# Optimization experiments

Measured on AMD Instinct MI355X. Metric: run time of the kernel, lower is better.

## Reference

```python
import jax, jax.numpy as jnp
import numpy as np
import math

B, S, H = 2, 2048, 2048
NQ, NKV, HD = 16, 4, 128
THETA = 10000.0


def rotate_half(x):
    x1, x2 = jnp.split(x, 2, axis=-1)
    return jnp.concatenate([-x2, x1], axis=-1)


def rope_cos_sin(position_ids, dim, base, dtype):
    # inv_freq: (dim/2,)
    inv_freq = 1.0 / (base ** (jnp.arange(0, dim, 2, dtype=jnp.float32) / dim))
    freqs = position_ids.astype(jnp.float32)[..., None] * inv_freq  # (B, S, dim/2)
    emb = jnp.concatenate([freqs, freqs], axis=-1)  # (B, S, dim)
    return jnp.cos(emb).astype(dtype), jnp.sin(emb).astype(dtype)


def setup_inputs() -> dict:
    key = jax.random.key(0)
    ks = jax.random.split(key, 5)
    hidden_states = jax.random.normal(ks[0], (B, S, H), dtype=jnp.float32)
    position_ids = jnp.broadcast_to(jnp.arange(S, dtype=jnp.int32)[None, :], (B, S))
    sc = 0.02
    wq = jax.random.normal(ks[1], (NQ * HD, H), dtype=jnp.float32) * sc
    wk = jax.random.normal(ks[2], (NKV * HD, H), dtype=jnp.float32) * sc
    wv = jax.random.normal(ks[3], (NKV * HD, H), dtype=jnp.float32) * sc
    wo = jax.random.normal(ks[4], (H, NQ * HD), dtype=jnp.float32) * sc
    return {"hidden_states": hidden_states, "position_ids": position_ids,
            "wq": wq, "wk": wk, "wv": wv, "wo": wo}


def reference(hidden_states, position_ids, wq, wk, wv, wo):
    b, s, _ = hidden_states.shape
    n_rep = NQ // NKV
    # QKV projections (no bias)
    q = (hidden_states @ wq.T).reshape(b, s, NQ, HD).transpose(0, 2, 1, 3)   # (b, nq, s, hd)
    k = (hidden_states @ wk.T).reshape(b, s, NKV, HD).transpose(0, 2, 1, 3)  # (b, nkv, s, hd)
    v = (hidden_states @ wv.T).reshape(b, s, NKV, HD).transpose(0, 2, 1, 3)
    # RoPE (full rotary, partial_rotary_factor == 1.0)
    cos, sin = rope_cos_sin(position_ids, HD, THETA, q.dtype)  # (b, s, hd)
    cos = cos[:, None, :, :]
    sin = sin[:, None, :, :]
    q = q * cos + rotate_half(q) * sin
    k = k * cos + rotate_half(k) * sin
    # repeat_kv for GQA: (b, nkv, s, hd) -> (b, nq, s, hd)
    k = jnp.repeat(k, n_rep, axis=1)
    v = jnp.repeat(v, n_rep, axis=1)
    # scores (b, nq, s, s)
    scores = jnp.einsum('bhqd,bhkd->bhqk', q, k) / math.sqrt(HD)
    causal = jnp.triu(jnp.full((s, s), -jnp.inf, dtype=scores.dtype), k=1)
    scores = scores + causal
    probs = jax.nn.softmax(scores.astype(jnp.float32), axis=-1).astype(q.dtype)
    out = jnp.einsum('bhqk,bhkd->bhqd', probs, v)  # (b, nq, s, hd)
    out = out.transpose(0, 2, 1, 3).reshape(b, s, NQ * HD)
    return out @ wo.T
```

## Files before the change

kernel.cpp:

```cpp
#include <hip/hip_runtime.h>
#include <hip/hip_bf16.h>
#include <cstdint>

typedef unsigned short u16;
typedef __attribute__((ext_vector_type(4))) float f32x4;
typedef __attribute__((ext_vector_type(8))) short s16x8;
typedef __attribute__((ext_vector_type(4))) unsigned int u32x4;
typedef __attribute__((ext_vector_type(2))) unsigned int u32x2;
typedef __attribute__((ext_vector_type(4))) unsigned short u16x4;
typedef __attribute__((ext_vector_type(8))) unsigned short u16x8;

#define MFMA16(a, b, c) __builtin_amdgcn_mfma_f32_16x16x32_bf16(a, b, c, 0, 0, 0)
#define GLOAD16(g, l) __builtin_amdgcn_global_load_lds((const __attribute__((address_space(1))) void*)(g), (__attribute__((address_space(3))) void*)(l), 16, 0, 0)

__device__ __forceinline__ u16 f2bf(float f) {
    union { float f; uint32_t u; } v{f};
    uint32_t r = v.u + 0x7FFF + ((v.u >> 16) & 1);
    return (u16)(r >> 16);
}
__device__ __forceinline__ float bf2f(u16 b) {
    union { uint32_t u; float f; } v;
    v.u = ((uint32_t)b) << 16;
    return v.f;
}

__global__ void cast_all(const float* __restrict__ h, const float* __restrict__ wq,
                         const float* __restrict__ wk, const float* __restrict__ wv,
                         const float* __restrict__ wo, const int* __restrict__ pos,
                         u16* __restrict__ Xb, u16* __restrict__ WB, u16* __restrict__ WoB,
                         float* __restrict__ ct, float* __restrict__ st) {
    if (blockIdx.x >= 18432) {
        int i = (blockIdx.x - 18432) * 256 + threadIdx.x;
        int j = i & 63;
        int bs = i >> 6;
        float p = (float)pos[bs];
        float invf = powf(10000.0f, -(float)j * (1.0f / 64.0f));
        float ang = p * invf;
        ct[i] = cosf(ang);
        st[i] = sinf(ang);
        return;
    }
    int i = blockIdx.x * 256 + threadIdx.x;
    const float* src; u16* dst; int off;
    if (i < 2097152)      { src = h;  dst = Xb;           off = i; }
    else if (i < 3145728) { src = wq; dst = WB;           off = i - 2097152; }
    else if (i < 3407872) { src = wk; dst = WB + 4194304; off = i - 3145728; }
    else if (i < 3670016) { src = wv; dst = WB + 5242880; off = i - 3407872; }
    else                  { src = wo; dst = WoB;          off = i - 3670016; }
    float4 f = ((const float4*)src)[off];
    u16x4 o = { f2bf(f.x), f2bf(f.y), f2bf(f.z), f2bf(f.w) };
    ((u16x4*)dst)[off] = o;
}

template <int FUSE>
__global__ __launch_bounds__(256) void gemm_bt(const u16* __restrict__ A, const u16* __restrict__ Bw,
                                               float* __restrict__ C, int M, int N, int K,
                                               const float* __restrict__ ct, const float* __restrict__ st,
                                               u16* __restrict__ Qb, u16* __restrict__ Kb,
                                               u16* __restrict__ Vb) {
    __shared__ u16 Sh[32768];
    const int tid = threadIdx.x;
    const int lane = tid & 63, wid = tid >> 6;
    const int g = lane >> 4, r = lane & 15;

    const int gx = gridDim.x, nwg = gx * gridDim.y;
    int lid = blockIdx.y * gx + blockIdx.x;
    int swz = (lid % 8) * (nwg / 8) + lid / 8;
    const int bxi = swz % gx, byi = swz / gx;

    const size_t bm = (size_t)byi * 128, bn = (size_t)bxi * 128;
    const int wr = (wid >> 1) * 64, wc = (wid & 1) * 64;

    const int srow = wid * 32 + (lane >> 3);
    const int schunk = (lane & 7) ^ ((lane >> 3) & 7);
    const u16* aSrc = A + (bm + srow) * (size_t)K + schunk * 8;
    const u16* bSrc = Bw + (bn + srow) * (size_t)K + schunk * 8;

    auto STAGE = [&](int ktEl, int bi) {
        u16* aD = Sh + bi * 16384 + wid * 2048;
        u16* bD = Sh + bi * 16384 + 8192 + wid * 2048;
#pragma unroll
        for (int j = 0; j < 4; ++j) {
            GLOAD16(aSrc + (size_t)(j * 8) * K + ktEl, aD + j * 512);
            GLOAD16(bSrc + (size_t)(j * 8) * K + ktEl, bD + j * 512);
        }
    };

    f32x4 acc[4][4] = {};
    const int nk = K >> 6;
    STAGE(0, 0);
    __syncthreads();
    for (int t = 0; t < nk; ++t) {
        if (t + 1 < nk) STAGE((t + 1) << 6, (t + 1) & 1);
        const u16* As = Sh + (t & 1) * 16384;
        const u16* Bs = As + 8192;
        s16x8 af[4][2], bfr[4][2];
#pragma unroll
        for (int m = 0; m < 4; ++m)
#pragma unroll
            for (int kk = 0; kk < 2; ++kk) {
                int rowa = wr + m * 16 + r;
                af[m][kk] = *(const s16x8*)(As + rowa * 64 + (((kk * 4 + g) ^ (rowa & 7)) << 3));
                int rowb = wc + m * 16 + r;
                bfr[m][kk] = *(const s16x8*)(Bs + rowb * 64 + (((kk * 4 + g) ^ (rowb & 7)) << 3));
            }
#pragma unroll
        for (int m = 0; m < 4; ++m)
#pragma unroll
            for (int n = 0; n < 4; ++n) {
                acc[m][n] = MFMA16(af[m][0], bfr[n][0], acc[m][n]);
                acc[m][n] = MFMA16(af[m][1], bfr[n][1], acc[m][n]);
            }
        __syncthreads();
    }
    if (FUSE == 0) {
#pragma unroll
        for (int m = 0; m < 4; ++m)
#pragma unroll
            for (int n = 0; n < 4; ++n)
#pragma unroll
                for (int i = 0; i < 4; ++i) {
                    size_t row = bm + wr + m * 16 + g * 4 + i;
                    size_t col = bn + wc + n * 16 + r;
                    C[row * N + col] = acc[m][n][i];
                }
        return;
    }
    const int hb = bxi;
    if (hb < 20) {
#pragma unroll
        for (int m = 0; m < 4; ++m)
#pragma unroll
            for (int n = 0; n < 4; ++n)
#pragma unroll
                for (int i = 0; i < 4; ++i) {
                    int rowl = wr + m * 16 + g * 4 + i;
                    int col = wc + n * 16 + r;
                    int c4 = col >> 3;
                    *(u16*)((char*)Sh + rowl * 256 + (((c4 ^ (rowl & 15))) << 4) + ((col & 7) << 1)) =
                        f2bf(acc[m][n][i]);
                }
        __syncthreads();
        if (tid < 128) {
            const int rowl = tid;
            const size_t tok = bm + rowl;
            const int b = (int)(tok >> 11), s = (int)(tok & 2047);
            u16* dst;
            if (hb < 16) dst = Qb + (((size_t)(b * 16 + hb) * 2048 + s) << 7);
            else         dst = Kb + (((size_t)(b * 4 + (hb - 16)) * 2048 + s) << 7);
            const char* tb = (const char*)Sh + rowl * 256;
            const float* ctr = ct + tok * 64;
            const float* str = st + tok * 64;
#pragma unroll
            for (int c4 = 0; c4 < 8; ++c4) {
                u32x4 lo4 = *(const u32x4*)(tb + ((c4 ^ (rowl & 15)) << 4));
                u32x4 hi4 = *(const u32x4*)(tb + (((c4 + 8) ^ (rowl & 15)) << 4));
                const u16* lo = (const u16*)&lo4;
                const u16* hi = (const u16*)&hi4;
                u16x4 o0, o1, o2, o3;
                u16* olo[2] = { (u16*)&o0, (u16*)&o1 };
                u16* ohi[2] = { (u16*)&o2, (u16*)&o3 };
#pragma unroll
                for (int j = 0; j < 8; ++j) {
                    float c = ctr[c4 * 8 + j], sn = str[c4 * 8 + j];
                    float xl = bf2f(lo[j]), xh = bf2f(hi[j]);
                    olo[j >> 2][j & 3] = f2bf(xl * c - xh * sn);
                    ohi[j >> 2][j & 3] = f2bf(xh * c + xl * sn);
                }
                *(u16x4*)(dst + c4 * 8) = o0;
                *(u16x4*)(dst + c4 * 8 + 4) = o1;
                *(u16x4*)(dst + 64 + c4 * 8) = o2;
                *(u16x4*)(dst + 64 + c4 * 8 + 4) = o3;
            }
        }
    } else {
#pragma unroll
        for (int m = 0; m < 4; ++m) {
            int tokb = wr + m * 16 + g * 4;
            int chunk = tokb >> 3;
            int sub = (g & 1) * 8;
#pragma unroll
            for (int n = 0; n < 4; ++n) {
                int d = wc + n * 16 + r;
                u16x4 v = { f2bf(acc[m][n][0]), f2bf(acc[m][n][1]),
                            f2bf(acc[m][n][2]), f2bf(acc[m][n][3]) };
                *(u16x4*)((char*)Sh + d * 256 + (((chunk ^ (d & 15))) << 4) + sub) = v;
            }
        }
        __syncthreads();
        const int b = (int)(bm >> 11), s0 = (int)(bm & 2047);
        u16* dst = Vb + (size_t)(b * 4 + (hb - 20)) * 262144;
        const int dd = tid >> 1, half = (tid & 1) * 8;
#pragma unroll
        for (int c8 = 0; c8 < 8; ++c8) {
            int sc = half + c8;
            u32x4 v4 = *(const u32x4*)((const char*)Sh + dd * 256 + (((sc ^ (dd & 15))) << 4));
            *(u32x4*)(dst + (size_t)dd * 2048 + s0 + sc * 8) = v4;
        }
    }
}

__global__ __launch_bounds__(256, 2) void attn_k(const u16* __restrict__ Qb, const u16* __restrict__ Kb,
                                                 const u16* __restrict__ Vb, u16* __restrict__ Ob) {
    __shared__ char smem[65536];
    u16* Vts = (u16*)(smem + 32768);
    char* Pall = smem + 49152;
    const int tid = threadIdx.x;
    const int lane = tid & 63, w = tid >> 6;
    const int g = lane >> 4, r = lane & 15;

    const int lid = blockIdx.y * gridDim.x + blockIdx.x;
    const int cpy = lid >> 8, p = lid & 255;
    const int bh = p & 31;
    const int qblk = cpy ? (7 - (p >> 5)) : ((p >> 5) + 8);

    const int b = bh >> 4, h = bh & 15;
    const int hkv = h >> 2;
    const int q0 = qblk * 128;
    const u16* Qh = Qb + ((size_t)(b * 16 + h) << 18);
    const u16* Kh = Kb + ((size_t)(b * 4 + hkv) << 18);
    const u16* Vh = Vb + ((size_t)(b * 4 + hkv) << 18);

    s16x8 qf[2][4];
#pragma unroll
    for (int qq = 0; qq < 2; ++qq)
#pragma unroll
        for (int c = 0; c < 4; ++c)
            qf[qq][c] = *(const s16x8*)(Qh + (size_t)(q0 + qq * 64 + w * 16 + r) * 128 + c * 32 + g * 8);

    f32x4 o[2][8] = {};
    float mrun[2] = {-1e30f, -1e30f};
    float lrun[2] = {0.f, 0.f};
    const int fmax[2] = { q0 + w * 16 + 15, q0 + 64 + w * 16 + 15 };

    const int ntiles = 2 * qblk + 2;
    const int krow0 = tid >> 4, kch = tid & 15;

    u32x4 kpr[4], vpr[4];
#pragma unroll
    for (int it = 0; it < 4; ++it)
        kpr[it] = *(const u32x4*)(Kh + (size_t)(krow0 + it * 16) * 128 + kch * 8);
#pragma unroll
    for (int it = 0; it < 4; ++it) {
        int task = tid + it * 256;
        vpr[it] = *(const u32x4*)(Vh + (size_t)(task >> 3) * 2048 + (task & 7) * 8);
    }
#pragma unroll
    for (int it = 0; it < 4; ++it) {
        int row = krow0 + it * 16;
        *(u32x4*)(smem + row * 256 + ((kch ^ (row & 7)) << 4)) = kpr[it];
    }
#pragma unroll
    for (int it = 0; it < 4; ++it) {
        int task = tid + it * 256;
        int d = task >> 3, ch = task & 7;
        *(u32x4*)((char*)Vts + d * 128 + ((ch ^ (d & 7) ^ ((d >> 3) & 7)) << 4)) = vpr[it];
    }
    if (ntiles > 1) {
#pragma unroll
        for (int it = 0; it < 4; ++it)
            kpr[it] = *(const u32x4*)(Kh + (size_t)(64 + krow0 + it * 16) * 128 + kch * 8);
#pragma unroll
        for (int it = 0; it < 4; ++it) {
            int task = tid + it * 256;
            vpr[it] = *(const u32x4*)(Vh + (size_t)(task >> 3) * 2048 + 64 + (task & 7) * 8);
        }
    }
    __syncthreads();

    for (int t = 0; t < ntiles; ++t) {
        const int kv0 = t * 64;
        const char* kb = smem + ((t & 1) << 14);
        f32x4 st4[2][4];
#pragma unroll
        for (int ts = 0; ts < 4; ++ts) {
            int row = ts * 16 + r;
            s16x8 kf[4];
#pragma unroll
            for (int c = 0; c < 4; ++c)
                kf[c] = *(const s16x8*)(kb + row * 256 + (((c * 4 + g) ^ (row & 7)) << 4));
            f32x4 a0 = {}, a1 = {};
            if (kv0 <= fmax[0])
#pragma unroll
                for (int c = 0; c < 4; ++c) a0 = MFMA16(kf[c], qf[0][c], a0);
            if (kv0 <= fmax[1])
#pragma unroll
                for (int c = 0; c < 4; ++c) a1 = MFMA16(kf[c], qf[1][c], a1);
            st4[0][ts] = a0;
            st4[1][ts] = a1;
        }
#pragma unroll
        for (int qq = 0; qq < 2; ++qq) {
            if (kv0 > fmax[qq]) continue;
            const int qg = q0 + qq * 64 + w * 16 + r;
            float sv[16];
            float mtile = -1e30f;
#pragma unroll
            for (int ts = 0; ts < 4; ++ts)
#pragma unroll
                for (int i = 0; i < 4; ++i) {
                    int kvg = kv0 + ts * 16 + g * 4 + i;
                    float s = st4[qq][ts][i] * 0.08838834764831845f;
                    s = (kvg > qg) ? -1e30f : s;
                    sv[ts * 4 + i] = s;
                    mtile = fmaxf(mtile, s);
                }
            mtile = fmaxf(mtile, __shfl_xor(mtile, 16));
            mtile = fmaxf(mtile, __shfl_xor(mtile, 32));
            float mold = mrun[qq];
            if (!__all(mtile <= mold + 8.0f)) {
                float mnew = fmaxf(mold, mtile);
                float corr = __expf(mold - mnew);
#pragma unroll
                for (int dsb = 0; dsb < 8; ++dsb)
#pragma unroll
                    for (int i = 0; i < 4; ++i) o[qq][dsb][i] *= corr;
                lrun[qq] *= corr;
                mrun[qq] = mnew;
            }
            float mm = mrun[qq];
            float psum = 0.f;
            unsigned int pw[8];
#pragma unroll
            for (int ts = 0; ts < 4; ++ts) {
                float p0 = __expf(sv[ts * 4 + 0] - mm);
                float p1 = __expf(sv[ts * 4 + 1] - mm);
                float p2 = __expf(sv[ts * 4 + 2] - mm);
                float p3 = __expf(sv[ts * 4 + 3] - mm);
                psum += (p0 + p1) + (p2 + p3);
                pw[ts * 2 + 0] = (unsigned int)f2bf(p0) | ((unsigned int)f2bf(p1) << 16);
                pw[ts * 2 + 1] = (unsigned int)f2bf(p2) | ((unsigned int)f2bf(p3) << 16);
            }
            psum += __shfl_xor(psum, 16);
            psum += __shfl_xor(psum, 32);
            lrun[qq] += psum;
            char* pbase = Pall + (w * 2 + qq) * 2048;
#pragma unroll
            for (int ts = 0; ts < 4; ++ts) {
                int chunk = (ts * 2 + (g >> 1)) ^ (r & 7);
                u32x2 val = { pw[ts * 2], pw[ts * 2 + 1] };
                *(u32x2*)(pbase + r * 128 + chunk * 16 + (g & 1) * 8) = val;
            }
        }
        asm volatile("s_waitcnt lgkmcnt(0)" ::: "memory");
        if (t + 1 < ntiles) {
            char* kbn = smem + (((t + 1) & 1) << 14);
#pragma unroll
            for (int it = 0; it < 4; ++it) {
                int row = krow0 + it * 16;
                *(u32x4*)(kbn + row * 256 + ((kch ^ (row & 7)) << 4)) = kpr[it];
            }
            if (t + 2 < ntiles) {
                const int kn2 = kv0 + 128;
#pragma unroll
                for (int it = 0; it < 4; ++it)
                    kpr[it] = *(const u32x4*)(Kh + (size_t)(kn2 + krow0 + it * 16) * 128 + kch * 8);
            }
        }
#pragma unroll
        for (int c = 0; c < 2; ++c) {
            s16x8 vf[8];
#pragma unroll
            for (int dsb = 0; dsb < 8; ++dsb) {
                int d = dsb * 16 + r;
                vf[dsb] = *(const s16x8*)((const char*)Vts + d * 128 +
                    ((((c * 4 + g) ^ (d & 7) ^ ((d >> 3) & 7))) << 4));
            }
#pragma unroll
            for (int qq = 0; qq < 2; ++qq) {
                if (kv0 > fmax[qq]) continue;
                s16x8 pf = *(const s16x8*)(Pall + (w * 2 + qq) * 2048 + r * 128 +
                                           (((c * 4 + g) ^ (r & 7)) << 4));
#pragma unroll
                for (int dsb = 0; dsb < 8; ++dsb)
                    o[qq][dsb] = MFMA16(vf[dsb], pf, o[qq][dsb]);
            }
        }
        __syncthreads();
        if (t + 1 < ntiles) {
#pragma unroll
            for (int it = 0; it < 4; ++it) {
                int task = tid + it * 256;
                int d = task >> 3, ch = task & 7;
                *(u32x4*)((char*)Vts + d * 128 + ((ch ^ (d & 7) ^ ((d >> 3) & 7)) << 4)) = vpr[it];
            }
            if (t + 2 < ntiles) {
                const int kn2 = kv0 + 128;
#pragma unroll
                for (int it = 0; it < 4; ++it) {
                    int task = tid + it * 256;
                    vpr[it] = *(const u32x4*)(Vh + (size_t)(task >> 3) * 2048 + kn2 + (task & 7) * 8);
                }
            }
        }
        __syncthreads();
    }
#pragma unroll
    for (int qq = 0; qq < 2; ++qq) {
        float linv = 1.0f / lrun[qq];
        char* obase = smem + (w << 13) + (qq << 12);
#pragma unroll
        for (int dsb = 0; dsb < 8; ++dsb)
#pragma unroll
            for (int i = 0; i < 4; ++i) {
                int d = dsb * 16 + g * 4 + i;
                *(u16*)(obase + r * 256 + d * 2) = f2bf(o[qq][dsb][i] * linv);
            }
    }
    asm volatile("s_waitcnt lgkmcnt(0)" ::: "memory");
    const int rr = lane >> 2, cbo = (lane & 3) * 32;
#pragma unroll
    for (int qq = 0; qq < 2; ++qq) {
        char* obase = smem + (w << 13) + (qq << 12);
        size_t oidx = ((size_t)b * 2048 + q0 + qq * 64 + w * 16 + rr) * 2048 + h * 128 + cbo;
#pragma unroll
        for (int p2 = 0; p2 < 4; ++p2) {
            u32x4 vv = *(const u32x4*)(obase + rr * 256 + cbo * 2 + p2 * 16);
            *(u32x4*)(Ob + oidx + p2 * 8) = vv;
        }
    }
}

extern "C" void kernel_launch(void* const* d_in, const int* in_sizes, int n_in,
                              void* d_out, int out_size, void* d_ws, size_t ws_size,
                              hipStream_t stream) {
    const float* hidden = (const float*)d_in[0];
    const int* pos = (const int*)d_in[1];
    const float* wq = (const float*)d_in[2];
    const float* wk = (const float*)d_in[3];
    const float* wv = (const float*)d_in[4];
    const float* wo = (const float*)d_in[5];
    float* out = (float*)d_out;

    char* ws = (char*)d_ws;
    size_t off = 0;
    auto alloc = [&](size_t bytes) { char* p = ws + off; off += (bytes + 255) & ~255ULL; return p; };
    u16* Xb   = (u16*)alloc(8388608ULL * 2);
    u16* WB   = (u16*)alloc(6291456ULL * 2);
    u16* WoB  = (u16*)alloc(4194304ULL * 2);
    u16* Qb   = (u16*)alloc(8388608ULL * 2);
    u16* Kb   = (u16*)alloc(2097152ULL * 2);
    u16* Vb   = (u16*)alloc(2097152ULL * 2);
    u16* Ab   = (u16*)alloc(8388608ULL * 2);
    float* ctab = (float*)alloc(262144ULL * 4);
    float* stab = (float*)alloc(262144ULL * 4);

    cast_all<<<19456, 256, 0, stream>>>(hidden, wq, wk, wv, wo, pos, Xb, WB, WoB, ctab, stab);
    gemm_bt<1><<<dim3(24, 32), 256, 0, stream>>>(Xb, WB, nullptr, 4096, 3072, 2048,
                                                 ctab, stab, Qb, Kb, Vb);
    attn_k<<<dim3(16, 32), 256, 0, stream>>>(Qb, Kb, Vb, Ab);
    gemm_bt<0><<<dim3(16, 32), 256, 0, stream>>>(Ab, WoB, out, 4096, 2048, 2048,
                                                 nullptr, nullptr, nullptr, nullptr, nullptr);
}
```

Measured before the change: 229.4 us.

## Enlarge attention blocks to 512 threads covering 256 query rows

The attention kernel now runs 8 waves per block, each block covering 256 query rows instead of 128. Each K/V tile staged in shared memory is therefore reused by twice as many query rows, and the grid is halved to 256 blocks. The P·V step is moved inside the per-query-group loop, so V fragments are re-read from LDS for each group, and the next K-tile store is interleaved into that loop. The old scheme pairing complementary causal query blocks for load balance is dropped, so blocks now differ widely in the number of KV tiles they process, and occupancy drops to one block per CU.

```diff
diff --git a/kernel.cpp b/kernel.cpp
--- a/kernel.cpp
+++ b/kernel.cpp
@@ -200,7 +200,7 @@
     }
 }
 
-__global__ __launch_bounds__(256, 2) void attn_k(const u16* __restrict__ Qb, const u16* __restrict__ Kb,
+__global__ __launch_bounds__(512, 1) void attn_k(const u16* __restrict__ Qb, const u16* __restrict__ Kb,
                                                  const u16* __restrict__ Vb, u16* __restrict__ Ob) {
     __shared__ char smem[65536];
     u16* Vts = (u16*)(smem + 32768);
@@ -210,59 +210,60 @@
     const int g = lane >> 4, r = lane & 15;
 
     const int lid = blockIdx.y * gridDim.x + blockIdx.x;
-    const int cpy = lid >> 8, p = lid & 255;
-    const int bh = p & 31;
-    const int qblk = cpy ? (7 - (p >> 5)) : ((p >> 5) + 8);
+    const int bh = lid & 31;
+    const int qblk = 7 - (lid >> 5);
 
     const int b = bh >> 4, h = bh & 15;
     const int hkv = h >> 2;
-    const int q0 = qblk * 128;
+    const int q0 = qblk * 256;
     const u16* Qh = Qb + ((size_t)(b * 16 + h) << 18);
     const u16* Kh = Kb + ((size_t)(b * 4 + hkv) << 18);
     const u16* Vh = Vb + ((size_t)(b * 4 + hkv) << 18);
 
+    const int base0 = q0 + w * 16, base1 = q0 + 128 + w * 16;
+    const int fmax[2] = { base0 + 15, base1 + 15 };
+
     s16x8 qf[2][4];
 #pragma unroll
-    for (int qq = 0; qq < 2; ++qq)
-#pragma unroll
-        for (int c = 0; c < 4; ++c)
-            qf[qq][c] = *(const s16x8*)(Qh + (size_t)(q0 + qq * 64 + w * 16 + r) * 128 + c * 32 + g * 8);
+    for (int c = 0; c < 4; ++c) {
+        qf[0][c] = *(const s16x8*)(Qh + (size_t)(base0 + r) * 128 + c * 32 + g * 8);
+        qf[1][c] = *(const s16x8*)(Qh + (size_t)(base1 + r) * 128 + c * 32 + g * 8);
+    }
 
     f32x4 o[2][8] = {};
     float mrun[2] = {-1e30f, -1e30f};
     float lrun[2] = {0.f, 0.f};
-    const int fmax[2] = { q0 + w * 16 + 15, q0 + 64 + w * 16 + 15 };
-
-    const int ntiles = 2 * qblk + 2;
+
+    const int ntiles = 4 * qblk + 4;
     const int krow0 = tid >> 4, kch = tid & 15;
 
-    u32x4 kpr[4], vpr[4];
-#pragma unroll
-    for (int it = 0; it < 4; ++it)
-        kpr[it] = *(const u32x4*)(Kh + (size_t)(krow0 + it * 16) * 128 + kch * 8);
-#pragma unroll
-    for (int it = 0; it < 4; ++it) {
-        int task = tid + it * 256;
+    u32x4 kpr[2], vpr[2];
+#pragma unroll
+    for (int it = 0; it < 2; ++it)
+        kpr[it] = *(const u32x4*)(Kh + (size_t)(krow0 + it * 32) * 128 + kch * 8);
+#pragma unroll
+    for (int it = 0; it < 2; ++it) {
+        int task = tid + it * 512;
         vpr[it] = *(const u32x4*)(Vh + (size_t)(task >> 3) * 2048 + (task & 7) * 8);
     }
 #pragma unroll
-    for (int it = 0; it < 4; ++it) {
-        int row = krow0 + it * 16;
+    for (int it = 0; it < 2; ++it) {
+        int row = krow0 + it * 32;
         *(u32x4*)(smem + row * 256 + ((kch ^ (row & 7)) << 4)) = kpr[it];
     }
 #pragma unroll
-    for (int it = 0; it < 4; ++it) {
-        int task = tid + it * 256;
+    for (int it = 0; it < 2; ++it) {
+        int task = tid + it * 512;
         int d = task >> 3, ch = task & 7;
         *(u32x4*)((char*)Vts + d * 128 + ((ch ^ (d & 7) ^ ((d >> 3) & 7)) << 4)) = vpr[it];
     }
     if (ntiles > 1) {
 #pragma unroll
-        for (int it = 0; it < 4; ++it)
-            kpr[it] = *(const u32x4*)(Kh + (size_t)(64 + krow0 + it * 16) * 128 + kch * 8);
-#pragma unroll
-        for (int it = 0; it < 4; ++it) {
-            int task = tid + it * 256;
+        for (int it = 0; it < 2; ++it)
+            kpr[it] = *(const u32x4*)(Kh + (size_t)(64 + krow0 + it * 32) * 128 + kch * 8);
+#pragma unroll
+        for (int it = 0; it < 2; ++it) {
+            int task = tid + it * 512;
             vpr[it] = *(const u32x4*)(Vh + (size_t)(task >> 3) * 2048 + 64 + (task & 7) * 8);
         }
     }
@@ -291,104 +292,97 @@
         }
 #pragma unroll
         for (int qq = 0; qq < 2; ++qq) {
-            if (kv0 > fmax[qq]) continue;
-            const int qg = q0 + qq * 64 + w * 16 + r;
-            float sv[16];
-            float mtile = -1e30f;
-#pragma unroll
-            for (int ts = 0; ts < 4; ++ts)
-#pragma unroll
-                for (int i = 0; i < 4; ++i) {
-                    int kvg = kv0 + ts * 16 + g * 4 + i;
-                    float s = st4[qq][ts][i] * 0.08838834764831845f;
-                    s = (kvg > qg) ? -1e30f : s;
-                    sv[ts * 4 + i] = s;
-                    mtile = fmaxf(mtile, s);
-                }
-            mtile = fmaxf(mtile, __shfl_xor(mtile, 16));
-            mtile = fmaxf(mtile, __shfl_xor(mtile, 32));
-            float mold = mrun[qq];
-            if (!__all(mtile <= mold + 8.0f)) {
-                float mnew = fmaxf(mold, mtile);
-                float corr = __expf(mold - mnew);
-#pragma unroll
-                for (int dsb = 0; dsb < 8; ++dsb)
-#pragma unroll
-                    for (int i = 0; i < 4; ++i) o[qq][dsb][i] *= corr;
-                lrun[qq] *= corr;
-                mrun[qq] = mnew;
-            }
-            float mm = mrun[qq];
-            float psum = 0.f;
-            unsigned int pw[8];
-#pragma unroll
-            for (int ts = 0; ts < 4; ++ts) {
-                float p0 = __expf(sv[ts * 4 + 0] - mm);
-                float p1 = __expf(sv[ts * 4 + 1] - mm);
-                float p2 = __expf(sv[ts * 4 + 2] - mm);
-                float p3 = __expf(sv[ts * 4 + 3] - mm);
-                psum += (p0 + p1) + (p2 + p3);
-                pw[ts * 2 + 0] = (unsigned int)f2bf(p0) | ((unsigned int)f2bf(p1) << 16);
-                pw[ts * 2 + 1] = (unsigned int)f2bf(p2) | ((unsigned int)f2bf(p3) << 16);
-            }
-            psum += __shfl_xor(psum, 16);
-            psum += __shfl_xor(psum, 32);
-            lrun[qq] += psum;
-            char* pbase = Pall + (w * 2 + qq) * 2048;
-#pragma unroll
-            for (int ts = 0; ts < 4; ++ts) {
-                int chunk = (ts * 2 + (g >> 1)) ^ (r & 7);
-                u32x2 val = { pw[ts * 2], pw[ts * 2 + 1] };
-                *(u32x2*)(pbase + r * 128 + chunk * 16 + (g & 1) * 8) = val;
-            }
-        }
-        asm volatile("s_waitcnt lgkmcnt(0)" ::: "memory");
+            if (kv0 <= fmax[qq]) {
+                const int qg = (qq ? base1 : base0) + r;
+                float sv[16];
+                float mtile = -1e30f;
+#pragma unroll
+                for (int ts = 0; ts < 4; ++ts)
+#pragma unroll
+                    for (int i = 0; i < 4; ++i) {
+                        int kvg = kv0 + ts * 16 + g * 4 + i;
+                        float s = st4[qq][ts][i] * 0.08838834764831845f;
+                        s = (kvg > qg) ? -1e30f : s;
+                        sv[ts * 4 + i] = s;
+                        mtile = fmaxf(mtile, s);
+                    }
+                mtile = fmaxf(mtile, __shfl_xor(mtile, 16));
+                mtile = fmaxf(mtile, __shfl_xor(mtile, 32));
+                float mold = mrun[qq];
+                if (!__all(mtile <= mold + 8.0f)) {
+                    float mnew = fmaxf(mold, mtile);
+                    float corr = __expf(mold - mnew);
+#pragma unroll
+                    for (int dsb = 0; dsb < 8; ++dsb)
+#pragma unroll
+                        for (int i = 0; i < 4; ++i) o[qq][dsb][i] *= corr;
+                    lrun[qq] *= corr;
+                    mrun[qq] = mnew;
+                }
+                float mm = mrun[qq];
+                float psum = 0.f;
+                unsigned int pw[8];
+#pragma unroll
+                for (int ts = 0; ts < 4; ++ts) {
+                    float p0 = __expf(sv[ts * 4 + 0] - mm);
+                    float p1 = __expf(sv[ts * 4 + 1] - mm);
+                    float p2 = __expf(sv[ts * 4 + 2] - mm);
+                    float p3 = __expf(sv[ts * 4 + 3] - mm);
+                    psum += (p0 + p1) + (p2 + p3);
+                    pw[ts * 2 + 0] = (unsigned int)f2bf(p0) | ((unsigned int)f2bf(p1) << 16);
+                    pw[ts * 2 + 1] = (unsigned int)f2bf(p2) | ((unsigned int)f2bf(p3) << 16);
+                }
+                psum += __shfl_xor(psum, 16);
+                psum += __shfl_xor(psum, 32);
+                lrun[qq] += psum;
+                char* pbase = Pall + w * 2048;
+#pragma unroll
+                for (int ts = 0; ts < 4; ++ts) {
+                    int chunk = (ts * 2 + (g >> 1)) ^ (r & 7);
+                    u32x2 val = { pw[ts * 2], pw[ts * 2 + 1] };
+                    *(u32x2*)(pbase + r * 128 + chunk * 16 + (g & 1) * 8) = val;
+                }
+                asm volatile("s_waitcnt lgkmcnt(0)" ::: "memory");
+#pragma unroll
+                for (int c = 0; c < 2; ++c) {
+                    s16x8 pf = *(const s16x8*)(pbase + r * 128 + (((c * 4 + g) ^ (r & 7)) << 4));
+#pragma unroll
+                    for (int dsb = 0; dsb < 8; ++dsb) {
+                        int d = dsb * 16 + r;
+                        s16x8 vf = *(const s16x8*)((const char*)Vts + d * 128 +
+                            ((((c * 4 + g) ^ (d & 7) ^ ((d >> 3) & 7))) << 4));
+                        o[qq][dsb] = MFMA16(vf, pf, o[qq][dsb]);
+                    }
+                }
+            }
+            if (qq == 0 && t + 1 < ntiles) {
+                char* kbn = smem + (((t + 1) & 1) << 14);
+#pragma unroll
+                for (int it = 0; it < 2; ++it) {
+                    int row = krow0 + it * 32;
+                    *(u32x4*)(kbn + row * 256 + ((kch ^ (row & 7)) << 4)) = kpr[it];
+                }
+                if (t + 2 < ntiles) {
+                    const int kn2 = kv0 + 128;
+#pragma unroll
+                    for (int it = 0; it < 2; ++it)
+                        kpr[it] = *(const u32x4*)(Kh + (size_t)(kn2 + krow0 + it * 32) * 128 + kch * 8);
+                }
+            }
+        }
+        __syncthreads();
         if (t + 1 < ntiles) {
-            char* kbn = smem + (((t + 1) & 1) << 14);
-#pragma unroll
-            for (int it = 0; it < 4; ++it) {
-                int row = krow0 + it * 16;
-                *(u32x4*)(kbn + row * 256 + ((kch ^ (row & 7)) << 4)) = kpr[it];
+#pragma unroll
+            for (int it = 0; it < 2; ++it) {
+                int task = tid + it * 512;
+                int d = task >> 3, ch = task & 7;
+                *(u32x4*)((char*)Vts + d * 128 + ((ch ^ (d & 7) ^ ((d >> 3) & 7)) << 4)) = vpr[it];
             }
             if (t + 2 < ntiles) {
                 const int kn2 = kv0 + 128;
 #pragma unroll
-                for (int it = 0; it < 4; ++it)
-                    kpr[it] = *(const u32x4*)(Kh + (size_t)(kn2 + krow0 + it * 16) * 128 + kch * 8);
-            }
-        }
-#pragma unroll
-        for (int c = 0; c < 2; ++c) {
-            s16x8 vf[8];
-#pragma unroll
-            for (int dsb = 0; dsb < 8; ++dsb) {
-                int d = dsb * 16 + r;
-                vf[dsb] = *(const s16x8*)((const char*)Vts + d * 128 +
-                    ((((c * 4 + g) ^ (d & 7) ^ ((d >> 3) & 7))) << 4));
-            }
-#pragma unroll
-            for (int qq = 0; qq < 2; ++qq) {
-                if (kv0 > fmax[qq]) continue;
-                s16x8 pf = *(const s16x8*)(Pall + (w * 2 + qq) * 2048 + r * 128 +
-                                           (((c * 4 + g) ^ (r & 7)) << 4));
-#pragma unroll
-                for (int dsb = 0; dsb < 8; ++dsb)
-                    o[qq][dsb] = MFMA16(vf[dsb], pf, o[qq][dsb]);
-            }
-        }
-        __syncthreads();
-        if (t + 1 < ntiles) {
-#pragma unroll
-            for (int it = 0; it < 4; ++it) {
-                int task = tid + it * 256;
-                int d = task >> 3, ch = task & 7;
-                *(u32x4*)((char*)Vts + d * 128 + ((ch ^ (d & 7) ^ ((d >> 3) & 7)) << 4)) = vpr[it];
-            }
-            if (t + 2 < ntiles) {
-                const int kn2 = kv0 + 128;
-#pragma unroll
-                for (int it = 0; it < 4; ++it) {
-                    int task = tid + it * 256;
+                for (int it = 0; it < 2; ++it) {
+                    int task = tid + it * 512;
                     vpr[it] = *(const u32x4*)(Vh + (size_t)(task >> 3) * 2048 + kn2 + (task & 7) * 8);
                 }
             }
@@ -398,7 +392,7 @@
 #pragma unroll
     for (int qq = 0; qq < 2; ++qq) {
         float linv = 1.0f / lrun[qq];
-        char* obase = smem + (w << 13) + (qq << 12);
+        char* obase = smem + (w * 2 + qq) * 4096;
 #pragma unroll
         for (int dsb = 0; dsb < 8; ++dsb)
 #pragma unroll
@@ -411,8 +405,9 @@
     const int rr = lane >> 2, cbo = (lane & 3) * 32;
 #pragma unroll
     for (int qq = 0; qq < 2; ++qq) {
-        char* obase = smem + (w << 13) + (qq << 12);
-        size_t oidx = ((size_t)b * 2048 + q0 + qq * 64 + w * 16 + rr) * 2048 + h * 128 + cbo;
+        char* obase = smem + (w * 2 + qq) * 4096;
+        const int baseq = qq ? base1 : base0;
+        size_t oidx = ((size_t)b * 2048 + baseq + rr) * 2048 + h * 128 + cbo;
 #pragma unroll
         for (int p2 = 0; p2 < 4; ++p2) {
             u32x4 vv = *(const u32x4*)(obase + rr * 256 + cbo * 2 + p2 * 16);
@@ -448,7 +443,7 @@
     cast_all<<<19456, 256, 0, stream>>>(hidden, wq, wk, wv, wo, pos, Xb, WB, WoB, ctab, stab);
     gemm_bt<1><<<dim3(24, 32), 256, 0, stream>>>(Xb, WB, nullptr, 4096, 3072, 2048,
                                                  ctab, stab, Qb, Kb, Vb);
-    attn_k<<<dim3(16, 32), 256, 0, stream>>>(Qb, Kb, Vb, Ab);
+    attn_k<<<dim3(8, 32), 512, 0, stream>>>(Qb, Kb, Vb, Ab);
     gemm_bt<0><<<dim3(16, 32), 256, 0, stream>>>(Ab, WoB, out, 4096, 2048, 2048,
                                                  nullptr, nullptr, nullptr, nullptr, nullptr);
 }
```

Result: slower. 252.1 us (+9.9%).
